# Kernel tuning notes

Hardware: AMD Instinct MI355X
Metric: run time of the kernel (lower is better)

The kernel has to match this reference:

```python
import jax, jax.numpy as jnp
import numpy as np

B, S, E, H, BS = 4, 4096, 1024, 1024, 128  # batch, seq, embed, head_size, block_size


def setup_inputs() -> dict:
    key = jax.random.key(0)
    k1, k2, k3, k4 = jax.random.split(key, 4)
    x = jax.random.normal(k1, (B, S, E), dtype=jnp.float32)
    W_qkv = jax.random.normal(k2, (E, 3 * H), dtype=jnp.float32) * (E ** -0.5)
    W_out = jax.random.normal(k3, (H, H), dtype=jnp.float32) * (H ** -0.5)
    b_out = jax.random.normal(k4, (H,), dtype=jnp.float32) * 0.01
    return {"x": x, "W_qkv": W_qkv, "W_out": W_out, "b_out": b_out}


def reference(x, W_qkv, W_out, b_out):
    b, s, e = x.shape
    h = W_out.shape[1]
    nb = s // BS  # number of blocks (block-diagonal attention)
    qkv = x @ W_qkv                      # [B, S, 3H]
    q, k, v = jnp.split(qkv, 3, axis=-1)

    def blk(t):
        return t.reshape(b, nb, BS, h)   # [B, nb, BS, H]

    scale = h ** -0.5
    # each query block attends only its own key/value block
    scores = jnp.einsum('bnqd,bnkd->bnqk', blk(q), blk(k)) * scale  # [B, nb, BS, BS]
    causal = jnp.tril(jnp.ones((BS, BS), dtype=bool))  # diagonal block of full tril
    scores = jnp.where(causal, scores, -jnp.inf)
    scores = scores - jnp.max(scores, axis=-1, keepdims=True)
    p = jnp.exp(scores)
    p = p / (jnp.sum(p, axis=-1, keepdims=True) + 1e-6)  # faithful: softmax with +1e-6 eps
    out = jnp.einsum('bnqk,bnkd->bnqd', p, blk(v)).reshape(b, s, h)
    return out @ W_out.T + b_out
```

## Files before the change

kernel.cpp:

```cpp
#include <hip/hip_runtime.h>
#include <hip/hip_bf16.h>

typedef __attribute__((ext_vector_type(8))) short short8;
typedef __attribute__((ext_vector_type(4))) float float4_;

typedef const __attribute__((address_space(1))) void* gas_t;
typedef __attribute__((address_space(3))) void* las_t;

__device__ __forceinline__ void gl_lds16(const void* g, void* l) {
  __builtin_amdgcn_global_load_lds((gas_t)g, (las_t)l, 16, 0, 0);
}

__device__ __forceinline__ short f2b(float f) {
  union { __hip_bfloat16 h; short s; } u;
  u.h = __float2bfloat16(f);
  return u.s;
}
__device__ __forceinline__ float b2f(short s) {
  union { short s; __hip_bfloat16 h; } u;
  u.s = s;
  return __bfloat162float(u.h);
}
__device__ __forceinline__ short8 cvt8(float4_ lo, float4_ hi) {
  short8 r;
#pragma unroll
  for (int t = 0; t < 4; t++) { r[t] = f2b(lo[t]); r[t + 4] = f2b(hi[t]); }
  return r;
}

__global__ __launch_bounds__(256) void f32_to_b16(
    const float* __restrict__ in, short* __restrict__ out, long n)
{
  const long i = ((long)blockIdx.x * 256 + threadIdx.x) * 8;
  if (i >= n) return;
  float4_ lo = *(const float4_*)&in[i];
  float4_ hi = *(const float4_*)&in[i + 4];
  *(short8*)&out[i] = cvt8(lo, hi);
}

__global__ __launch_bounds__(256) void transpose64(
    const float* __restrict__ in, short* __restrict__ out, int R, int C)
{
  __shared__ __align__(16) short T[64 * 72];
  const int tid = threadIdx.x;
  const int r0 = blockIdx.y * 64;
  const int c0 = blockIdx.x * 64;
  const int r  = tid >> 2;
  const int cp = (tid & 3) * 16;
#pragma unroll
  for (int g = 0; g < 4; g++) {
    float4_ v = *(const float4_*)&in[(long)(r0 + r) * C + c0 + cp + g * 4];
#pragma unroll
    for (int t = 0; t < 4; t++) T[(cp + g * 4 + t) * 72 + r] = f2b(v[t]);
  }
  __syncthreads();
  const int c  = tid >> 2;
  const int rp = (tid & 3) * 16;
  short8 w0 = *(const short8*)&T[c * 72 + rp];
  short8 w1 = *(const short8*)&T[c * 72 + rp + 8];
  *(short8*)&out[(long)(c0 + c) * R + r0 + rp] = w0;
  *(short8*)&out[(long)(c0 + c) * R + r0 + rp + 8] = w1;
}

__global__ __launch_bounds__(256) void gemm_bt(
    const void* __restrict__ Av, int lda, int a_f32,
    const short* __restrict__ B,
    void* __restrict__ Cv, int ldc, int c_f32,
    int K, const float* __restrict__ bias)
{
  __shared__ __align__(16) short As[128 * 32];
  __shared__ __align__(16) short Bs[128 * 32];
  const int tid  = threadIdx.x;
  const int lane = tid & 63;
  const int w    = tid >> 6;
  const int quad = lane >> 4;
  const int l15  = lane & 15;
  const int wm   = (w >> 1) * 64;
  const int wn   = (w & 1) * 64;
  const int m0   = blockIdx.y * 128;
  const int n0   = blockIdx.x * 128;
  const int wbase = w * 512;

  float4_ acc[4][4] = {};

  const int srow = tid >> 2;
  const int kp   = (tid & 3) * 8;

  for (int k0 = 0; k0 < K; k0 += 32) {
    short8 a_lo, a_hi;
    if (a_f32) {
      const float* Af = (const float*)Av;
      float4_ l0 = *(const float4_*)&Af[(long)(m0 + srow) * lda + k0 + kp];
      float4_ l1 = *(const float4_*)&Af[(long)(m0 + srow) * lda + k0 + kp + 4];
      float4_ h0 = *(const float4_*)&Af[(long)(m0 + srow + 64) * lda + k0 + kp];
      float4_ h1 = *(const float4_*)&Af[(long)(m0 + srow + 64) * lda + k0 + kp + 4];
      a_lo = cvt8(l0, l1);
      a_hi = cvt8(h0, h1);
    }
    __syncthreads();
    if (a_f32) {
      *(short8*)&As[srow * 32 + kp]        = a_lo;
      *(short8*)&As[(srow + 64) * 32 + kp] = a_hi;
    } else {
      const short* Ab = (const short*)Av;
      gl_lds16(&Ab[(long)(m0 + srow) * lda + k0 + kp],      &As[wbase]);
      gl_lds16(&Ab[(long)(m0 + srow + 64) * lda + k0 + kp], &As[2048 + wbase]);
    }
    gl_lds16(&B[(long)(n0 + srow) * K + k0 + kp],      &Bs[wbase]);
    gl_lds16(&B[(long)(n0 + srow + 64) * K + k0 + kp], &Bs[2048 + wbase]);
    __syncthreads();
    short8 a[4], b[4];
#pragma unroll
    for (int i = 0; i < 4; i++)
      a[i] = *(const short8*)&As[(wm + i * 16 + l15) * 32 + quad * 8];
#pragma unroll
    for (int j = 0; j < 4; j++)
      b[j] = *(const short8*)&Bs[(wn + j * 16 + l15) * 32 + quad * 8];
#pragma unroll
    for (int i = 0; i < 4; i++)
#pragma unroll
      for (int j = 0; j < 4; j++)
        acc[i][j] = __builtin_amdgcn_mfma_f32_16x16x32_bf16(a[i], b[j], acc[i][j], 0, 0, 0);
  }

#pragma unroll
  for (int i = 0; i < 4; i++) {
    const int rm = m0 + wm + i * 16 + quad * 4;
#pragma unroll
    for (int j = 0; j < 4; j++) {
      const int cn = n0 + wn + j * 16 + l15;
      if (c_f32) {
        float* C = (float*)Cv;
        const float bv = bias ? bias[cn] : 0.0f;
#pragma unroll
        for (int r = 0; r < 4; r++)
          C[(long)(rm + r) * ldc + cn] = acc[i][j][r] + bv;
      } else {
        short* C = (short*)Cv;
#pragma unroll
        for (int r = 0; r < 4; r++)
          C[(long)(rm + r) * ldc + cn] = f2b(acc[i][j][r]);
      }
    }
  }
}

__global__ __launch_bounds__(256) void attn_blockdiag(short* __restrict__ qkv)
{
  __shared__ __align__(16) short Qs[128 * 32];
  __shared__ __align__(16) short Ks[128 * 32];
  __shared__ __align__(16) short Ps[128 * 136];
  __shared__ __align__(16) short Vt[64 * 136];

  const int tid  = threadIdx.x;
  const int lane = tid & 63;
  const int w    = tid >> 6;
  const int quad = lane >> 4;
  const int l15  = lane & 15;
  const long base = (long)blockIdx.x * 128 * 3072;
  const int wbase = w * 512;

  float4_ acc[2][8] = {};
  const int srow = tid >> 2;
  const int kp   = (tid & 3) * 8;
  const short* Qg = qkv + base;
  const short* Kg = qkv + base + 1024;

  for (int k0 = 0; k0 < 1024; k0 += 32) {
    __syncthreads();
    gl_lds16(&Qg[(long)srow * 3072 + k0 + kp],        &Qs[wbase]);
    gl_lds16(&Qg[(long)(srow + 64) * 3072 + k0 + kp], &Qs[2048 + wbase]);
    gl_lds16(&Kg[(long)srow * 3072 + k0 + kp],        &Ks[wbase]);
    gl_lds16(&Kg[(long)(srow + 64) * 3072 + k0 + kp], &Ks[2048 + wbase]);
    __syncthreads();
    short8 a0 = *(const short8*)&Qs[(w * 32 + l15) * 32 + quad * 8];
    short8 a1 = *(const short8*)&Qs[(w * 32 + 16 + l15) * 32 + quad * 8];
#pragma unroll
    for (int j = 0; j < 8; j++) {
      short8 b = *(const short8*)&Ks[(j * 16 + l15) * 32 + quad * 8];
      acc[0][j] = __builtin_amdgcn_mfma_f32_16x16x32_bf16(a0, b, acc[0][j], 0, 0, 0);
      acc[1][j] = __builtin_amdgcn_mfma_f32_16x16x32_bf16(a1, b, acc[1][j], 0, 0, 0);
    }
  }
  __syncthreads();

  const float scale = 0.03125f;
#pragma unroll
  for (int i = 0; i < 2; i++) {
#pragma unroll
    for (int r = 0; r < 4; r++) {
      const int rowq = w * 32 + i * 16 + quad * 4 + r;
      float s[8];
      float mx = -3.0e38f;
#pragma unroll
      for (int j = 0; j < 8; j++) {
        const int col = j * 16 + l15;
        const float v = acc[i][j][r] * scale;
        s[j] = (col <= rowq) ? v : -3.0e38f;
        mx = fmaxf(mx, s[j]);
      }
      mx = fmaxf(mx, __shfl_xor(mx, 1));
      mx = fmaxf(mx, __shfl_xor(mx, 2));
      mx = fmaxf(mx, __shfl_xor(mx, 4));
      mx = fmaxf(mx, __shfl_xor(mx, 8));
      float p[8];
      float sum = 0.0f;
#pragma unroll
      for (int j = 0; j < 8; j++) {
        p[j] = (s[j] > -1.0e38f) ? __expf(s[j] - mx) : 0.0f;
        sum += p[j];
      }
      sum += __shfl_xor(sum, 1);
      sum += __shfl_xor(sum, 2);
      sum += __shfl_xor(sum, 4);
      sum += __shfl_xor(sum, 8);
      const float inv = 1.0f / (sum + 1e-6f);
#pragma unroll
      for (int j = 0; j < 8; j++)
        Ps[rowq * 136 + j * 16 + l15] = f2b(p[j] * inv);
    }
  }

  const short* Vg = qkv + base + 2048;
  short* Op = qkv + base;
  const int kr = tid >> 1;
  const int dp = (tid & 1) * 32;

  for (int d0 = 0; d0 < 1024; d0 += 64) {
    __syncthreads();
#pragma unroll
    for (int g = 0; g < 4; g++) {
      short8 v = *(const short8*)&Vg[(long)kr * 3072 + d0 + dp + g * 8];
#pragma unroll
      for (int t = 0; t < 8; t++)
        Vt[(dp + g * 8 + t) * 136 + kr] = v[t];
    }
    __syncthreads();

    float4_ o[2][4] = {};
#pragma unroll
    for (int kk = 0; kk < 4; kk++) {
      short8 a0 = *(const short8*)&Ps[(w * 32 + l15) * 136 + kk * 32 + quad * 8];
      short8 a1 = *(const short8*)&Ps[(w * 32 + 16 + l15) * 136 + kk * 32 + quad * 8];
      const int kb = kk * 32 + quad * 8;
#pragma unroll
      for (int j = 0; j < 4; j++) {
        short8 b = *(const short8*)&Vt[(j * 16 + l15) * 136 + kb];
        o[0][j] = __builtin_amdgcn_mfma_f32_16x16x32_bf16(a0, b, o[0][j], 0, 0, 0);
        o[1][j] = __builtin_amdgcn_mfma_f32_16x16x32_bf16(a1, b, o[1][j], 0, 0, 0);
      }
    }
#pragma unroll
    for (int i = 0; i < 2; i++)
#pragma unroll
      for (int j = 0; j < 4; j++)
#pragma unroll
        for (int r = 0; r < 4; r++) {
          const int rq = w * 32 + i * 16 + quad * 4 + r;
          const int d  = d0 + j * 16 + l15;
          Op[(long)rq * 3072 + d] = f2b(o[i][j][r]);
        }
  }
}

extern "C" void kernel_launch(void* const* d_in, const int* in_sizes, int n_in,
                              void* d_out, int out_size, void* d_ws, size_t ws_size,
                              hipStream_t stream) {
  const float* x    = (const float*)d_in[0];
  const float* Wqkv = (const float*)d_in[1];
  const float* Wout = (const float*)d_in[2];
  const float* bout = (const float*)d_in[3];
  float* out = (float*)d_out;

  char* ws = (char*)d_ws;
  short* WqkvT = (short*)ws;
  short* Woutb = (short*)(ws + 6291456);
  short* qkv   = (short*)(ws + 8388608);
  short* xb    = (short*)(ws + 8388608 + (size_t)16384 * 3072 * 2);

  transpose64<<<dim3(48, 16), 256, 0, stream>>>(Wqkv, WqkvT, 1024, 3072);
  f32_to_b16<<<512, 256, 0, stream>>>(Wout, Woutb, 1048576L);

  if (ws_size >= 8388608 + (size_t)16384 * 3072 * 2 + (size_t)16384 * 1024 * 2) {
    f32_to_b16<<<8192, 256, 0, stream>>>(x, xb, 16777216L);
    gemm_bt<<<dim3(24, 128), 256, 0, stream>>>(xb, 1024, 0, WqkvT,
                                               qkv, 3072, 0, 1024, nullptr);
    attn_blockdiag<<<dim3(128), 256, 0, stream>>>(qkv);
    gemm_bt<<<dim3(8, 128), 256, 0, stream>>>(qkv, 3072, 0, Woutb,
                                              out, 1024, 1, 1024, bout);
  } else if (ws_size >= 8388608 + (size_t)16384 * 3072 * 2) {
    gemm_bt<<<dim3(24, 128), 256, 0, stream>>>(x, 1024, 1, WqkvT,
                                               qkv, 3072, 0, 1024, nullptr);
    attn_blockdiag<<<dim3(128), 256, 0, stream>>>(qkv);
    gemm_bt<<<dim3(8, 128), 256, 0, stream>>>(qkv, 3072, 0, Woutb,
                                              out, 1024, 1, 1024, bout);
  } else {
    for (int c = 0; c < 4; c++) {
      const float* xc = x + (long)c * 4096 * 1024;
      float* outc = out + (long)c * 4096 * 1024;
      gemm_bt<<<dim3(24, 32), 256, 0, stream>>>(xc, 1024, 1, WqkvT,
                                                qkv, 3072, 0, 1024, nullptr);
      attn_blockdiag<<<dim3(32), 256, 0, stream>>>(qkv);
      gemm_bt<<<dim3(8, 32), 256, 0, stream>>>(qkv, 3072, 0, Woutb,
                                               outc, 1024, 1, 1024, bout);
    }
  }
}
```

Measured before the change: 379.9 us.

## Split attention tiles across two causal half-blocks and coalesce epilogue stores via LDS

```diff
diff --git a/kernel.cpp b/kernel.cpp
--- a/kernel.cpp
+++ b/kernel.cpp
@@ -68,8 +68,7 @@
     void* __restrict__ Cv, int ldc, int c_f32,
     int K, const float* __restrict__ bias)
 {
-  __shared__ __align__(16) short As[128 * 32];
-  __shared__ __align__(16) short Bs[128 * 32];
+  __shared__ __align__(16) short smem[2 * 128 * 32];
   const int tid  = threadIdx.x;
   const int lane = tid & 63;
   const int w    = tid >> 6;
@@ -99,23 +98,23 @@
     }
     __syncthreads();
     if (a_f32) {
-      *(short8*)&As[srow * 32 + kp]        = a_lo;
-      *(short8*)&As[(srow + 64) * 32 + kp] = a_hi;
+      *(short8*)&smem[srow * 32 + kp]        = a_lo;
+      *(short8*)&smem[(srow + 64) * 32 + kp] = a_hi;
     } else {
       const short* Ab = (const short*)Av;
-      gl_lds16(&Ab[(long)(m0 + srow) * lda + k0 + kp],      &As[wbase]);
-      gl_lds16(&Ab[(long)(m0 + srow + 64) * lda + k0 + kp], &As[2048 + wbase]);
-    }
-    gl_lds16(&B[(long)(n0 + srow) * K + k0 + kp],      &Bs[wbase]);
-    gl_lds16(&B[(long)(n0 + srow + 64) * K + k0 + kp], &Bs[2048 + wbase]);
+      gl_lds16(&Ab[(long)(m0 + srow) * lda + k0 + kp],      &smem[wbase]);
+      gl_lds16(&Ab[(long)(m0 + srow + 64) * lda + k0 + kp], &smem[2048 + wbase]);
+    }
+    gl_lds16(&B[(long)(n0 + srow) * K + k0 + kp],      &smem[4096 + wbase]);
+    gl_lds16(&B[(long)(n0 + srow + 64) * K + k0 + kp], &smem[6144 + wbase]);
     __syncthreads();
     short8 a[4], b[4];
 #pragma unroll
     for (int i = 0; i < 4; i++)
-      a[i] = *(const short8*)&As[(wm + i * 16 + l15) * 32 + quad * 8];
+      a[i] = *(const short8*)&smem[(wm + i * 16 + l15) * 32 + quad * 8];
 #pragma unroll
     for (int j = 0; j < 4; j++)
-      b[j] = *(const short8*)&Bs[(wn + j * 16 + l15) * 32 + quad * 8];
+      b[j] = *(const short8*)&smem[4096 + (wn + j * 16 + l15) * 32 + quad * 8];
 #pragma unroll
     for (int i = 0; i < 4; i++)
 #pragma unroll
@@ -123,144 +122,184 @@
         acc[i][j] = __builtin_amdgcn_mfma_f32_16x16x32_bf16(a[i], b[j], acc[i][j], 0, 0, 0);
   }
 
-#pragma unroll
+  const int gidx = w >> 1;
   for (int i = 0; i < 4; i++) {
-    const int rm = m0 + wm + i * 16 + quad * 4;
-#pragma unroll
-    for (int j = 0; j < 4; j++) {
-      const int cn = n0 + wn + j * 16 + l15;
-      if (c_f32) {
-        float* C = (float*)Cv;
-        const float bv = bias ? bias[cn] : 0.0f;
-#pragma unroll
-        for (int r = 0; r < 4; r++)
-          C[(long)(rm + r) * ldc + cn] = acc[i][j][r] + bv;
-      } else {
-        short* C = (short*)Cv;
-#pragma unroll
-        for (int r = 0; r < 4; r++)
-          C[(long)(rm + r) * ldc + cn] = f2b(acc[i][j][r]);
-      }
-    }
-  }
-}
-
-__global__ __launch_bounds__(256) void attn_blockdiag(short* __restrict__ qkv)
-{
-  __shared__ __align__(16) short Qs[128 * 32];
-  __shared__ __align__(16) short Ks[128 * 32];
-  __shared__ __align__(16) short Ps[128 * 136];
-  __shared__ __align__(16) short Vt[64 * 136];
+    __syncthreads();
+    if (c_f32) {
+      float* scr = (float*)smem;
+#pragma unroll
+      for (int j = 0; j < 4; j++) {
+        const int col = wn + j * 16 + l15;
+        const float bv = bias ? bias[n0 + col] : 0.0f;
+#pragma unroll
+        for (int r = 0; r < 4; r++) {
+          const int row = gidx * 16 + quad * 4 + r;
+          scr[row * 128 + (col ^ ((row & 7) << 4))] = acc[i][j][r] + bv;
+        }
+      }
+    } else {
+#pragma unroll
+      for (int j = 0; j < 4; j++) {
+        const int col = wn + j * 16 + l15;
+#pragma unroll
+        for (int r = 0; r < 4; r++) {
+          const int row = gidx * 16 + quad * 4 + r;
+          smem[row * 128 + (col ^ ((row & 7) << 4))] = f2b(acc[i][j][r]);
+        }
+      }
+    }
+    __syncthreads();
+    const int rs   = tid >> 3;
+    const int colp = (tid & 7) * 16;
+    const int cs   = colp ^ ((rs & 7) << 4);
+    const long row_g = m0 + (rs >> 4) * 64 + i * 16 + (rs & 15);
+    if (c_f32) {
+      float* C = (float*)Cv;
+      const float* scr = (const float*)smem;
+#pragma unroll
+      for (int q = 0; q < 4; q++) {
+        float4_ v = *(const float4_*)&scr[rs * 128 + cs + q * 4];
+        *(float4_*)&C[row_g * ldc + n0 + colp + q * 4] = v;
+      }
+    } else {
+      short* C = (short*)Cv;
+      short8 v0 = *(const short8*)&smem[rs * 128 + cs];
+      short8 v1 = *(const short8*)&smem[rs * 128 + cs + 8];
+      *(short8*)&C[row_g * ldc + n0 + colp]     = v0;
+      *(short8*)&C[row_g * ldc + n0 + colp + 8] = v1;
+    }
+  }
+}
+
+template<int NJ>
+__device__ __forceinline__ void attn_body(short* __restrict__ qkv, int tile,
+                                          short* smem)
+{
+  constexpr int NK    = NJ * 16;
+  constexpr int STR   = NK + 8;
+  constexpr int QROW0 = (NJ == 8) ? 64 : 0;
+  short* Qs = smem;
+  short* Ks = smem + 2048;
+  short* Ps = Ks + NK * 32;
+  short* Vt = Ps + 64 * STR;
+  short* Ot = Vt + 64 * STR;
 
   const int tid  = threadIdx.x;
   const int lane = tid & 63;
   const int w    = tid >> 6;
   const int quad = lane >> 4;
   const int l15  = lane & 15;
-  const long base = (long)blockIdx.x * 128 * 3072;
+  const long base = (long)tile * 128 * 3072;
   const int wbase = w * 512;
 
-  float4_ acc[2][8] = {};
+  const short* Qg = qkv + base + (long)QROW0 * 3072;
+  const short* Kg = qkv + base + 1024;
+  const short* Vg = qkv + base + 2048;
+
+  float4_ acc[NJ] = {};
   const int srow = tid >> 2;
   const int kp   = (tid & 3) * 8;
-  const short* Qg = qkv + base;
-  const short* Kg = qkv + base + 1024;
 
   for (int k0 = 0; k0 < 1024; k0 += 32) {
     __syncthreads();
-    gl_lds16(&Qg[(long)srow * 3072 + k0 + kp],        &Qs[wbase]);
-    gl_lds16(&Qg[(long)(srow + 64) * 3072 + k0 + kp], &Qs[2048 + wbase]);
-    gl_lds16(&Kg[(long)srow * 3072 + k0 + kp],        &Ks[wbase]);
-    gl_lds16(&Kg[(long)(srow + 64) * 3072 + k0 + kp], &Ks[2048 + wbase]);
-    __syncthreads();
-    short8 a0 = *(const short8*)&Qs[(w * 32 + l15) * 32 + quad * 8];
-    short8 a1 = *(const short8*)&Qs[(w * 32 + 16 + l15) * 32 + quad * 8];
-#pragma unroll
-    for (int j = 0; j < 8; j++) {
+    gl_lds16(&Qg[(long)srow * 3072 + k0 + kp], &Qs[wbase]);
+    gl_lds16(&Kg[(long)srow * 3072 + k0 + kp], &Ks[wbase]);
+    if (NJ == 8)
+      gl_lds16(&Kg[(long)(srow + 64) * 3072 + k0 + kp], &Ks[2048 + wbase]);
+    __syncthreads();
+    short8 a = *(const short8*)&Qs[(w * 16 + l15) * 32 + quad * 8];
+#pragma unroll
+    for (int j = 0; j < NJ; j++) {
       short8 b = *(const short8*)&Ks[(j * 16 + l15) * 32 + quad * 8];
-      acc[0][j] = __builtin_amdgcn_mfma_f32_16x16x32_bf16(a0, b, acc[0][j], 0, 0, 0);
-      acc[1][j] = __builtin_amdgcn_mfma_f32_16x16x32_bf16(a1, b, acc[1][j], 0, 0, 0);
-    }
-  }
-  __syncthreads();
+      acc[j] = __builtin_amdgcn_mfma_f32_16x16x32_bf16(a, b, acc[j], 0, 0, 0);
+    }
+  }
 
   const float scale = 0.03125f;
 #pragma unroll
-  for (int i = 0; i < 2; i++) {
-#pragma unroll
-    for (int r = 0; r < 4; r++) {
-      const int rowq = w * 32 + i * 16 + quad * 4 + r;
-      float s[8];
-      float mx = -3.0e38f;
-#pragma unroll
-      for (int j = 0; j < 8; j++) {
-        const int col = j * 16 + l15;
-        const float v = acc[i][j][r] * scale;
-        s[j] = (col <= rowq) ? v : -3.0e38f;
-        mx = fmaxf(mx, s[j]);
-      }
-      mx = fmaxf(mx, __shfl_xor(mx, 1));
-      mx = fmaxf(mx, __shfl_xor(mx, 2));
-      mx = fmaxf(mx, __shfl_xor(mx, 4));
-      mx = fmaxf(mx, __shfl_xor(mx, 8));
-      float p[8];
-      float sum = 0.0f;
-#pragma unroll
-      for (int j = 0; j < 8; j++) {
-        p[j] = (s[j] > -1.0e38f) ? __expf(s[j] - mx) : 0.0f;
-        sum += p[j];
-      }
-      sum += __shfl_xor(sum, 1);
-      sum += __shfl_xor(sum, 2);
-      sum += __shfl_xor(sum, 4);
-      sum += __shfl_xor(sum, 8);
-      const float inv = 1.0f / (sum + 1e-6f);
-#pragma unroll
-      for (int j = 0; j < 8; j++)
-        Ps[rowq * 136 + j * 16 + l15] = f2b(p[j] * inv);
-    }
-  }
-
-  const short* Vg = qkv + base + 2048;
-  short* Op = qkv + base;
-  const int kr = tid >> 1;
-  const int dp = (tid & 1) * 32;
-
+  for (int r = 0; r < 4; r++) {
+    const int rowq = w * 16 + quad * 4 + r;
+    float s[NJ];
+    float mx = -3.0e38f;
+#pragma unroll
+    for (int j = 0; j < NJ; j++) {
+      const int col = j * 16 + l15;
+      const float v = acc[j][r] * scale;
+      s[j] = (col <= QROW0 + rowq) ? v : -3.0e38f;
+      mx = fmaxf(mx, s[j]);
+    }
+    mx = fmaxf(mx, __shfl_xor(mx, 1));
+    mx = fmaxf(mx, __shfl_xor(mx, 2));
+    mx = fmaxf(mx, __shfl_xor(mx, 4));
+    mx = fmaxf(mx, __shfl_xor(mx, 8));
+    float p[NJ];
+    float sum = 0.0f;
+#pragma unroll
+    for (int j = 0; j < NJ; j++) {
+      p[j] = (s[j] > -1.0e38f) ? __expf(s[j] - mx) : 0.0f;
+      sum += p[j];
+    }
+    sum += __shfl_xor(sum, 1);
+    sum += __shfl_xor(sum, 2);
+    sum += __shfl_xor(sum, 4);
+    sum += __shfl_xor(sum, 8);
+    const float inv = 1.0f / (sum + 1e-6f);
+#pragma unroll
+    for (int j = 0; j < NJ; j++)
+      Ps[rowq * STR + j * 16 + l15] = f2b(p[j] * inv);
+  }
+
+  short* Op = qkv + base + (long)QROW0 * 3072;
   for (int d0 = 0; d0 < 1024; d0 += 64) {
     __syncthreads();
-#pragma unroll
-    for (int g = 0; g < 4; g++) {
-      short8 v = *(const short8*)&Vg[(long)kr * 3072 + d0 + dp + g * 8];
-#pragma unroll
-      for (int t = 0; t < 8; t++)
-        Vt[(dp + g * 8 + t) * 136 + kr] = v[t];
-    }
-    __syncthreads();
-
-    float4_ o[2][4] = {};
-#pragma unroll
-    for (int kk = 0; kk < 4; kk++) {
-      short8 a0 = *(const short8*)&Ps[(w * 32 + l15) * 136 + kk * 32 + quad * 8];
-      short8 a1 = *(const short8*)&Ps[(w * 32 + 16 + l15) * 136 + kk * 32 + quad * 8];
-      const int kb = kk * 32 + quad * 8;
+    if (NJ == 8) {
+      const int kr = tid >> 1, dp = (tid & 1) * 32;
+#pragma unroll
+      for (int gg = 0; gg < 4; gg++) {
+        short8 v = *(const short8*)&Vg[(long)kr * 3072 + d0 + dp + gg * 8];
+#pragma unroll
+        for (int t = 0; t < 8; t++) Vt[(dp + gg * 8 + t) * STR + kr] = v[t];
+      }
+    } else {
+      const int kr = tid >> 2, dp = (tid & 3) * 16;
+#pragma unroll
+      for (int gg = 0; gg < 2; gg++) {
+        short8 v = *(const short8*)&Vg[(long)kr * 3072 + d0 + dp + gg * 8];
+#pragma unroll
+        for (int t = 0; t < 8; t++) Vt[(dp + gg * 8 + t) * STR + kr] = v[t];
+      }
+    }
+    __syncthreads();
+    float4_ o[4] = {};
+#pragma unroll
+    for (int kk = 0; kk < NK / 32; kk++) {
+      short8 a = *(const short8*)&Ps[(w * 16 + l15) * STR + kk * 32 + quad * 8];
 #pragma unroll
       for (int j = 0; j < 4; j++) {
-        short8 b = *(const short8*)&Vt[(j * 16 + l15) * 136 + kb];
-        o[0][j] = __builtin_amdgcn_mfma_f32_16x16x32_bf16(a0, b, o[0][j], 0, 0, 0);
-        o[1][j] = __builtin_amdgcn_mfma_f32_16x16x32_bf16(a1, b, o[1][j], 0, 0, 0);
-      }
-    }
-#pragma unroll
-    for (int i = 0; i < 2; i++)
-#pragma unroll
-      for (int j = 0; j < 4; j++)
-#pragma unroll
-        for (int r = 0; r < 4; r++) {
-          const int rq = w * 32 + i * 16 + quad * 4 + r;
-          const int d  = d0 + j * 16 + l15;
-          Op[(long)rq * 3072 + d] = f2b(o[i][j][r]);
-        }
-  }
+        short8 b = *(const short8*)&Vt[(j * 16 + l15) * STR + kk * 32 + quad * 8];
+        o[j] = __builtin_amdgcn_mfma_f32_16x16x32_bf16(a, b, o[j], 0, 0, 0);
+      }
+    }
+#pragma unroll
+    for (int j = 0; j < 4; j++)
+#pragma unroll
+      for (int r = 0; r < 4; r++)
+        Ot[(w * 16 + quad * 4 + r) * 72 + j * 16 + l15] = f2b(o[j][r]);
+    __syncthreads();
+    const int orow = tid >> 2, ocp = (tid & 3) * 16;
+    short8 v0 = *(const short8*)&Ot[orow * 72 + ocp];
+    short8 v1 = *(const short8*)&Ot[orow * 72 + ocp + 8];
+    *(short8*)&Op[(long)orow * 3072 + d0 + ocp]     = v0;
+    *(short8*)&Op[(long)orow * 3072 + d0 + ocp + 8] = v1;
+  }
+}
+
+__global__ __launch_bounds__(256) void attn_blockdiag(short* __restrict__ qkv)
+{
+  __shared__ __align__(16) short smem[28160];
+  const int tile = blockIdx.x >> 1;
+  if (blockIdx.x & 1) attn_body<8>(qkv, tile, smem);
+  else                attn_body<4>(qkv, tile, smem);
 }
 
 extern "C" void kernel_launch(void* const* d_in, const int* in_sizes, int n_in,
@@ -285,13 +324,13 @@
     f32_to_b16<<<8192, 256, 0, stream>>>(x, xb, 16777216L);
     gemm_bt<<<dim3(24, 128), 256, 0, stream>>>(xb, 1024, 0, WqkvT,
                                                qkv, 3072, 0, 1024, nullptr);
-    attn_blockdiag<<<dim3(128), 256, 0, stream>>>(qkv);
+    attn_blockdiag<<<dim3(256), 256, 0, stream>>>(qkv);
     gemm_bt<<<dim3(8, 128), 256, 0, stream>>>(qkv, 3072, 0, Woutb,
                                               out, 1024, 1, 1024, bout);
   } else if (ws_size >= 8388608 + (size_t)16384 * 3072 * 2) {
     gemm_bt<<<dim3(24, 128), 256, 0, stream>>>(x, 1024, 1, WqkvT,
                                                qkv, 3072, 0, 1024, nullptr);
-    attn_blockdiag<<<dim3(128), 256, 0, stream>>>(qkv);
+    attn_blockdiag<<<dim3(256), 256, 0, stream>>>(qkv);
     gemm_bt<<<dim3(8, 128), 256, 0, stream>>>(qkv, 3072, 0, Woutb,
                                               out, 1024, 1, 1024, bout);
   } else {
@@ -300,7 +339,7 @@
       float* outc = out + (long)c * 4096 * 1024;
       gemm_bt<<<dim3(24, 32), 256, 0, stream>>>(xc, 1024, 1, WqkvT,
                                                 qkv, 3072, 0, 1024, nullptr);
-      attn_blockdiag<<<dim3(32), 256, 0, stream>>>(qkv);
+      attn_blockdiag<<<dim3(64), 256, 0, stream>>>(qkv);
       gemm_bt<<<dim3(8, 32), 256, 0, stream>>>(qkv, 3072, 0, Woutb,
                                                outc, 1024, 1, 1024, bout);
     }
```

Result: no change. 376.6 us (-0.9%).
